# Performance work log

Measured on AMD Instinct MI355X. Metric: run time of the kernel, lower is better.

The kernel has to match this reference:

```python
import jax, jax.numpy as jnp
import numpy as np

B, T, C, H = 8, 1024, 512, 8
EPS = 1e-5


def _layer_norm(x, g, b):
    m = jnp.mean(x, axis=-1, keepdims=True)
    v = jnp.var(x, axis=-1, keepdims=True)
    return (x - m) * jax.lax.rsqrt(v + EPS) * g + b


def setup_inputs() -> dict:
    key = jax.random.key(0)
    ks = jax.random.split(key, 6)
    s = 0.02  # init scale for weights
    return {
        "x": jax.random.normal(ks[0], (B, T, C), dtype=jnp.float32),
        # per-head full-width projections, stacked over heads: [H, C, C]
        "Wq": jax.random.normal(ks[1], (H, C, C), dtype=jnp.float32) * s,
        "bq": jnp.zeros((H, C), dtype=jnp.float32),
        "Wk": jax.random.normal(ks[2], (H, C, C), dtype=jnp.float32) * s,
        "bk": jnp.zeros((H, C), dtype=jnp.float32),
        "Wv": jax.random.normal(ks[3], (H, C, C), dtype=jnp.float32) * s,
        "bv": jnp.zeros((H, C), dtype=jnp.float32),
        # per-head LayerNorm params
        "ln_g": jnp.ones((H, C), dtype=jnp.float32),
        "ln_b": jnp.zeros((H, C), dtype=jnp.float32),
        # output projection: Linear(channels*heads, channels)
        "Wf": jax.random.normal(ks[4], (H * C, C), dtype=jnp.float32) * s,
        "bf": jnp.zeros((C,), dtype=jnp.float32),
    }


def reference(x, Wq, bq, Wk, bk, Wv, bv, ln_g, ln_b, Wf, bf):
    # Batched over heads: the torch code loops heads in Python; here one einsum.
    q = jnp.einsum('btc,hcd->bhtd', x, Wq) + bq[None, :, None, :]
    k = jnp.einsum('btc,hcd->bhtd', x, Wk) + bk[None, :, None, :]
    v = jnp.einsum('btc,hcd->bhtd', x, Wv) + bv[None, :, None, :]
    scale = 1.0 / np.sqrt(C).astype(np.float32)
    attn = jax.nn.softmax(jnp.einsum('bhtd,bhsd->bhts', q, k) * scale, axis=-1)
    z = jnp.einsum('bhts,bhsd->bhtd', attn, v)          # [B,H,T,C]
    z = _layer_norm(z, ln_g[None, :, None, :], ln_b[None, :, None, :])
    # concat heads along feature dim (matches torch.cat(results, dim=-1))
    zc = jnp.transpose(z, (0, 2, 1, 3)).reshape(B, T, H * C)
    out = zc @ Wf + bf + x                               # fc + residual
    return out
```

## Files before the change

kernel.cpp:

```cpp
#include <hip/hip_runtime.h>
#include <hip/hip_bf16.h>
#include <stdint.h>

typedef unsigned short u16;
typedef short s16x8 __attribute__((ext_vector_type(8)));
typedef float f32x4 __attribute__((ext_vector_type(4)));
typedef unsigned short u16x4 __attribute__((ext_vector_type(4)));
typedef unsigned short u16x8 __attribute__((ext_vector_type(8)));

#define B_ 8
#define T_ 1024
#define C_ 512
#define H_ 8
#define M_ (B_*T_)

__device__ __forceinline__ u16 f2bf(float f) {
  unsigned u = __builtin_bit_cast(unsigned, f);
  u += 0x7FFFu + ((u >> 16) & 1u);
  return (u16)(u >> 16);
}

__device__ __forceinline__ f32x4 mfma16(s16x8 a, s16x8 b, f32x4 c) {
  return __builtin_amdgcn_mfma_f32_16x16x32_bf16(a, b, c, 0, 0, 0);
}

__device__ __forceinline__ void glds16(const void* g, void* l) {
  __builtin_amdgcn_global_load_lds(
      (__attribute__((address_space(1))) const uint32_t*)g,
      (__attribute__((address_space(3))) uint32_t*)l, 16, 0, 0);
}

__global__ void cvt_x(const float* __restrict__ src, u16* __restrict__ dst, int n8) {
  int i = blockIdx.x * blockDim.x + threadIdx.x;
  if (i < n8) {
    float4 a = ((const float4*)src)[2*i];
    float4 b = ((const float4*)src)[2*i + 1];
    u16x8 o;
    o[0]=f2bf(a.x); o[1]=f2bf(a.y); o[2]=f2bf(a.z); o[3]=f2bf(a.w);
    o[4]=f2bf(b.x); o[5]=f2bf(b.y); o[6]=f2bf(b.z); o[7]=f2bf(b.w);
    ((u16x8*)dst)[i] = o;
  }
}

__global__ void transpose_f32_to_bf16(const float* __restrict__ src, u16* __restrict__ dst,
                                      int R, int Cc, long sstride, long dstride) {
  int nTc = Cc >> 5;
  int tr = (blockIdx.x / nTc) << 5;
  int tc = (blockIdx.x % nTc) << 5;
  src += (long)blockIdx.y * sstride;
  dst += (long)blockIdx.y * dstride;
  __shared__ float tile[32][33];
  int tx = threadIdx.x, ty = threadIdx.y;
  #pragma unroll
  for (int i = 0; i < 4; ++i) {
    int r = ty + i*8;
    tile[r][tx] = src[(long)(tr + r)*Cc + tc + tx];
  }
  __syncthreads();
  #pragma unroll
  for (int i = 0; i < 4; ++i) {
    int r = ty + i*8;
    dst[(long)(tc + r)*R + tr + tx] = f2bf(tile[tx][r]);
  }
}

#define STAGE_TILE(SRC, STRIDE, LDS)                                        \
  _Pragma("unroll")                                                         \
  for (int r_ = 0; r_ < 4; ++r_) {                                          \
    int o_ = r_*4096 + tid*16;                                              \
    int row_ = o_ >> 7, cb_ = o_ & 127;                                     \
    int cbs_ = cb_ ^ ((row_ & 7) << 4);                                     \
    glds16((SRC) + (size_t)row_*(STRIDE) + kofs + (cbs_ >> 1),              \
           (char*)(LDS) + r_*4096 + ((tid >> 6) << 10));                    \
  }

__global__ __launch_bounds__(256, 2) void gemm_qkv(
    const u16* __restrict__ xbf, const u16* __restrict__ wt,
    const float* __restrict__ bq, const float* __restrict__ bk, const float* __restrict__ bv,
    u16* __restrict__ qO, u16* __restrict__ kO, u16* __restrict__ vT,
    int h0, int lg)
{
  __shared__ u16 As[128*64];
  __shared__ u16 Bs[128*64];
  const int tid = threadIdx.x;
  const int lane = tid & 63, w = tid >> 6;
  const int wm = w >> 1, wn = w & 1;
  const int l15 = lane & 15, l4 = lane >> 4;
  const int by = blockIdx.y;
  const int p = by >> lg;
  const int hh = by & ((1 << lg) - 1);
  const int h = h0 + hh;
  const int ph = p*8 + h;
  const int mt = blockIdx.x >> 2, nt = blockIdx.x & 3;
  const int m0 = mt * 128, n0 = nt * 128;

  const u16* aSrc = xbf + (size_t)m0 * 512;
  const u16* bSrc = wt + ((size_t)ph * 512 + n0) * 512;

  f32x4 acc[4][4];
  #pragma unroll
  for (int i = 0; i < 4; ++i)
    #pragma unroll
    for (int j = 0; j < 4; ++j) acc[i][j] = f32x4{0.f,0.f,0.f,0.f};

  for (int kt = 0; kt < 8; ++kt) {
    const int kofs = kt * 64;
    STAGE_TILE(aSrc, 512, As);
    STAGE_TILE(bSrc, 512, Bs);
    __syncthreads();
    #pragma unroll
    for (int kk = 0; kk < 2; ++kk) {
      s16x8 af[4], bfr[4];
      #pragma unroll
      for (int i = 0; i < 4; ++i) {
        int rowA = wm*64 + i*16 + l15;
        af[i] = *(const s16x8*)((const char*)As + rowA*128 + ((kk*64 + l4*16) ^ ((rowA & 7) << 4)));
        int rowB = wn*64 + i*16 + l15;
        bfr[i] = *(const s16x8*)((const char*)Bs + rowB*128 + ((kk*64 + l4*16) ^ ((rowB & 7) << 4)));
      }
      #pragma unroll
      for (int i = 0; i < 4; ++i)
        #pragma unroll
        for (int j = 0; j < 4; ++j)
          acc[i][j] = mfma16(af[i], bfr[j], acc[i][j]);
    }
    __syncthreads();
  }

  const int dBase = n0 + wn*64;
  const int mBase = m0 + wm*64;
  if (p < 2) {
    const float* bias = (p == 0 ? bq : bk) + h*512;
    u16* outp = (p == 0 ? qO : kO) + (size_t)hh * M_ * 512;
    #pragma unroll
    for (int j = 0; j < 4; ++j) {
      int d = dBase + j*16 + l15;
      float bvs = bias[d];
      #pragma unroll
      for (int i = 0; i < 4; ++i) {
        int m = mBase + i*16 + l4*4;
        #pragma unroll
        for (int r = 0; r < 4; ++r)
          outp[(size_t)(m + r)*512 + d] = f2bf(acc[i][j][r] + bvs);
      }
    }
  } else {
    const float* bias = bv + h*512;
    #pragma unroll
    for (int j = 0; j < 4; ++j) {
      int d = dBase + j*16 + l15;
      float bvs = bias[d];
      #pragma unroll
      for (int i = 0; i < 4; ++i) {
        int m = mBase + i*16 + l4*4;
        int b_ = m >> 10, t0_ = m & 1023;
        u16x4 pk;
        #pragma unroll
        for (int r = 0; r < 4; ++r) pk[r] = f2bf(acc[i][j][r] + bvs);
        *(u16x4*)(vT + (((size_t)(hh*B_ + b_)*512 + d)*1024 + t0_)) = pk;
      }
    }
  }
}

__global__ __launch_bounds__(256, 2) void attn(
    const u16* __restrict__ qB, const u16* __restrict__ kB, const u16* __restrict__ vT,
    const float* __restrict__ lng, const float* __restrict__ lnb,
    u16* __restrict__ zO, int h0)
{
  __shared__ u16 Ks[32*512];
  __shared__ u16 Vs[512*40];
  __shared__ u16 Pl[4][512];
  const int tid = threadIdx.x;
  const int lane = tid & 63, w = tid >> 6;
  const int l15 = lane & 15, l4 = lane >> 4;

  const int Dd = blockIdx.x;
  const int xcd = Dd & 7, slot = Dd >> 3;
  const int gg = xcd + 8*(slot >> 4);
  const int qt = slot & 15;
  const int hg = gg >> 3, b = gg & 7;
  const int h = h0 + hg;
  const int t0 = qt*64 + w*16;
  const size_t hb = (size_t)hg*B_ + b;

  const u16* qP = qB + (hb*1024 + t0 + l15)*512 + l4*8;
  s16x8 qf[16];
  #pragma unroll
  for (int ks = 0; ks < 16; ++ks) qf[ks] = *(const s16x8*)(qP + ks*32);

  f32x4 z[32];
  #pragma unroll
  for (int df = 0; df < 32; ++df) z[df] = f32x4{0.f,0.f,0.f,0.f};
  float L = 0.f;
  const float c1 = 0.06376390696f;

  const u16* kBase = kB + hb*1024*512;
  const u16* vBase = vT + hb*512*1024;
  char* myP = (char*)&Pl[w][0];
  const int swz = (l15 & 3) << 4;
  const int kswz = (l15 & 7) << 4;

  for (int s0 = 0; s0 < 1024; s0 += 32) {
    #pragma unroll
    for (int it = 0; it < 8; ++it) {
      int o = it*4096 + tid*16;
      int row = o >> 10, cb = o & 1023;
      int cbs = cb ^ ((row & 7) << 4);
      glds16(kBase + (size_t)(s0 + row)*512 + (cbs >> 1),
             (char*)Ks + it*4096 + ((tid >> 6) << 10));
    }
    u16x8 vreg[8];
    #pragma unroll
    for (int it = 0; it < 8; ++it) {
      int r = (tid >> 2) + it*64;
      vreg[it] = *(const u16x8*)(vBase + (size_t)r*1024 + s0 + (tid & 3)*8);
    }
    #pragma unroll
    for (int it = 0; it < 8; ++it) {
      int r = (tid >> 2) + it*64;
      *(u16x8*)((char*)Vs + r*80 + (tid & 3)*16) = vreg[it];
    }
    __syncthreads();

    f32x4 sf0 = f32x4{0.f,0.f,0.f,0.f};
    f32x4 sf1 = f32x4{0.f,0.f,0.f,0.f};
    #pragma unroll
    for (int ks = 0; ks < 16; ++ks) {
      int col = (ks*64 + l4*16) ^ kswz;
      s16x8 k0 = *(const s16x8*)((const char*)Ks + l15*1024 + col);
      s16x8 k1 = *(const s16x8*)((const char*)Ks + (16 + l15)*1024 + col);
      sf0 = mfma16(k0, qf[ks], sf0);
      sf1 = mfma16(k1, qf[ks], sf1);
    }
    u16x4 p0, p1;
    #pragma unroll
    for (int r = 0; r < 4; ++r) {
      float e0 = exp2f(sf0[r] * c1);
      float e1 = exp2f(sf1[r] * c1);
      L += e0 + e1;
      p0[r] = f2bf(e0);
      p1[r] = f2bf(e1);
    }
    *(u16x4*)(myP + l15*64 + (( l4*8      ) ^ swz)) = p0;
    *(u16x4*)(myP + l15*64 + ((32 + l4*8  ) ^ swz)) = p1;
    s16x8 pb = *(const s16x8*)(myP + l15*64 + ((l4*16) ^ swz));

    #pragma unroll
    for (int df = 0; df < 32; ++df) {
      int d = df*16 + l15;
      s16x8 va = *(const s16x8*)((const char*)Vs + d*80 + l4*16);
      z[df] = mfma16(va, pb, z[df]);
    }
    __syncthreads();
  }

  L += __shfl_xor(L, 16);
  L += __shfl_xor(L, 32);
  float inv = 1.f / L;

  float s1 = 0.f, s2 = 0.f;
  #pragma unroll
  for (int df = 0; df < 32; ++df)
    #pragma unroll
    for (int r = 0; r < 4; ++r) {
      float v = z[df][r] * inv;
      z[df][r] = v;
      s1 += v; s2 += v*v;
    }
  s1 += __shfl_xor(s1, 16); s1 += __shfl_xor(s1, 32);
  s2 += __shfl_xor(s2, 16); s2 += __shfl_xor(s2, 32);
  const float mean = s1 * (1.f/512.f);
  const float var  = s2 * (1.f/512.f) - mean*mean;
  const float rstd = rsqrtf(var + 1e-5f);

  const float* gp = lng + h*512;
  const float* bp = lnb + h*512;
  u16* zp = zO + ((size_t)(b*1024 + t0 + l15))*4096 + h*512;
  #pragma unroll
  for (int df = 0; df < 32; ++df) {
    int d0 = df*16 + l4*4;
    float4 gv  = *(const float4*)(gp + d0);
    float4 bbv = *(const float4*)(bp + d0);
    u16x4 pk;
    pk[0] = f2bf((z[df][0]-mean)*rstd*gv.x + bbv.x);
    pk[1] = f2bf((z[df][1]-mean)*rstd*gv.y + bbv.y);
    pk[2] = f2bf((z[df][2]-mean)*rstd*gv.z + bbv.z);
    pk[3] = f2bf((z[df][3]-mean)*rstd*gv.w + bbv.w);
    *(u16x4*)(zp + d0) = pk;
  }
}

__global__ __launch_bounds__(256, 2) void gemm_fc(
    const u16* __restrict__ zb, const u16* __restrict__ wft,
    const float* __restrict__ bf_, const float* __restrict__ x,
    float* __restrict__ out)
{
  __shared__ u16 As[128*64];
  __shared__ u16 Bs[128*64];
  const int tid = threadIdx.x;
  const int lane = tid & 63, w = tid >> 6;
  const int wm = w >> 1, wn = w & 1;
  const int l15 = lane & 15, l4 = lane >> 4;
  const int mt = blockIdx.x >> 2, nt = blockIdx.x & 3;
  const int m0 = mt * 128, n0 = nt * 128;

  const u16* aSrc = zb + (size_t)m0 * 4096;
  const u16* bSrc = wft + (size_t)n0 * 4096;

  f32x4 acc[4][4];
  #pragma unroll
  for (int i = 0; i < 4; ++i)
    #pragma unroll
    for (int j = 0; j < 4; ++j) acc[i][j] = f32x4{0.f,0.f,0.f,0.f};

  for (int kt = 0; kt < 64; ++kt) {
    const int kofs = kt * 64;
    STAGE_TILE(aSrc, 4096, As);
    STAGE_TILE(bSrc, 4096, Bs);
    __syncthreads();
    #pragma unroll
    for (int kk = 0; kk < 2; ++kk) {
      s16x8 af[4], bfr[4];
      #pragma unroll
      for (int i = 0; i < 4; ++i) {
        int rowA = wm*64 + i*16 + l15;
        af[i] = *(const s16x8*)((const char*)As + rowA*128 + ((kk*64 + l4*16) ^ ((rowA & 7) << 4)));
        int rowB = wn*64 + i*16 + l15;
        bfr[i] = *(const s16x8*)((const char*)Bs + rowB*128 + ((kk*64 + l4*16) ^ ((rowB & 7) << 4)));
      }
      #pragma unroll
      for (int i = 0; i < 4; ++i)
        #pragma unroll
        for (int j = 0; j < 4; ++j)
          acc[i][j] = mfma16(af[i], bfr[j], acc[i][j]);
    }
    __syncthreads();
  }

  const int dBase = n0 + wn*64;
  const int mBase = m0 + wm*64;
  #pragma unroll
  for (int j = 0; j < 4; ++j) {
    int d = dBase + j*16 + l15;
    float bvs = bf_[d];
    #pragma unroll
    for (int i = 0; i < 4; ++i) {
      int m = mBase + i*16 + l4*4;
      #pragma unroll
      for (int r = 0; r < 4; ++r) {
        size_t idx = (size_t)(m + r)*512 + d;
        out[idx] = acc[i][j][r] + bvs + x[idx];
      }
    }
  }
}

extern "C" void kernel_launch(void* const* d_in, const int* in_sizes, int n_in,
                              void* d_out, int out_size, void* d_ws, size_t ws_size,
                              hipStream_t stream) {
  const float* x   = (const float*)d_in[0];
  const float* Wq  = (const float*)d_in[1];
  const float* bq  = (const float*)d_in[2];
  const float* Wk  = (const float*)d_in[3];
  const float* bk  = (const float*)d_in[4];
  const float* Wv  = (const float*)d_in[5];
  const float* bv  = (const float*)d_in[6];
  const float* lng = (const float*)d_in[7];
  const float* lnb = (const float*)d_in[8];
  const float* Wf  = (const float*)d_in[9];
  const float* bf_ = (const float*)d_in[10];
  float* out = (float*)d_out;

  char* ws = (char*)d_ws;
  u16* xbf = (u16*)(ws);
  u16* wt  = (u16*)(ws + 8388608);
  u16* wft = (u16*)(ws + 20971520);
  u16* zb  = (u16*)(ws + 25165824);

  const size_t headB = 8388608;
  const size_t base  = 92274688;
  int g, lg;
  if      (ws_size >= base + 24*headB) { g = 8; lg = 3; }
  else if (ws_size >= base + 12*headB) { g = 4; lg = 2; }
  else if (ws_size >= base +  6*headB) { g = 2; lg = 1; }
  else                                 { g = 1; lg = 0; }

  u16* qb = (u16*)(ws + base);
  u16* kb = (u16*)(ws + base + (size_t)g*headB);
  u16* vt = (u16*)(ws + base + (size_t)2*g*headB);

  cvt_x<<<2048, 256, 0, stream>>>(x, xbf, 524288);
  dim3 tb(32, 8);
  transpose_f32_to_bf16<<<dim3(256, 8), tb, 0, stream>>>(Wq, wt,             512, 512, 262144, 262144);
  transpose_f32_to_bf16<<<dim3(256, 8), tb, 0, stream>>>(Wk, wt +  8*262144, 512, 512, 262144, 262144);
  transpose_f32_to_bf16<<<dim3(256, 8), tb, 0, stream>>>(Wv, wt + 16*262144, 512, 512, 262144, 262144);
  transpose_f32_to_bf16<<<dim3(2048, 1), tb, 0, stream>>>(Wf, wft, 4096, 512, 0, 0);

  for (int h0 = 0; h0 < H_; h0 += g) {
    gemm_qkv<<<dim3(256, 3*g), 256, 0, stream>>>(xbf, wt, bq, bk, bv, qb, kb, vt, h0, lg);
    attn<<<dim3(128*g), 256, 0, stream>>>(qb, kb, vt, lng, lnb, zb, h0);
  }
  gemm_fc<<<256, 256, 0, stream>>>(zb, wft, bf_, x, out);
}
```

Measured before the change: 685.3 us.

## Double-buffer K/V tiles in attention with async global-to-LDS loads

Splits the K and V shared-memory tiles into two buffers and prefetches the next 32-key tile while the current one is consumed, leaving one barrier per iteration. V is now loaded with direct global-to-LDS copies using an XOR-swizzled layout instead of passing through registers into a padded layout. LDS use roughly doubles, so launch bounds drop to one block per SM, which lowers occupancy in exchange for overlapping memory with compute.

```diff
diff --git a/kernel.cpp b/kernel.cpp
--- a/kernel.cpp
+++ b/kernel.cpp
@@ -163,13 +163,13 @@
   }
 }
 
-__global__ __launch_bounds__(256, 2) void attn(
+__global__ __launch_bounds__(256, 1) void attn(
     const u16* __restrict__ qB, const u16* __restrict__ kB, const u16* __restrict__ vT,
     const float* __restrict__ lng, const float* __restrict__ lnb,
     u16* __restrict__ zO, int h0)
 {
-  __shared__ u16 Ks[32*512];
-  __shared__ u16 Vs[512*40];
+  __shared__ u16 Ks[2][32*512];
+  __shared__ u16 Vs[2][512*32];
   __shared__ u16 Pl[4][512];
   const int tid = threadIdx.x;
   const int lane = tid & 63, w = tid >> 6;
@@ -201,35 +201,44 @@
   const int swz = (l15 & 3) << 4;
   const int kswz = (l15 & 7) << 4;
 
-  for (int s0 = 0; s0 < 1024; s0 += 32) {
+  auto stageK = [&](int buf, int s0) {
     #pragma unroll
     for (int it = 0; it < 8; ++it) {
       int o = it*4096 + tid*16;
       int row = o >> 10, cb = o & 1023;
       int cbs = cb ^ ((row & 7) << 4);
       glds16(kBase + (size_t)(s0 + row)*512 + (cbs >> 1),
-             (char*)Ks + it*4096 + ((tid >> 6) << 10));
-    }
-    u16x8 vreg[8];
+             (char*)Ks[buf] + it*4096 + ((tid >> 6) << 10));
+    }
+  };
+  auto stageV = [&](int buf, int s0) {
     #pragma unroll
     for (int it = 0; it < 8; ++it) {
-      int r = (tid >> 2) + it*64;
-      vreg[it] = *(const u16x8*)(vBase + (size_t)r*1024 + s0 + (tid & 3)*8);
-    }
-    #pragma unroll
-    for (int it = 0; it < 8; ++it) {
-      int r = (tid >> 2) + it*64;
-      *(u16x8*)((char*)Vs + r*80 + (tid & 3)*16) = vreg[it];
-    }
-    __syncthreads();
+      int F = it*4096 + tid*16;
+      int d = F >> 6;
+      int cl = (F & 63) ^ (((d >> 1) & 3) << 4);
+      glds16(vBase + (size_t)d*1024 + s0 + (cl >> 1),
+             (char*)Vs[buf] + it*4096 + ((tid >> 6) << 10));
+    }
+  };
+
+  stageK(0, 0);
+  stageV(0, 0);
+  __syncthreads();
+
+  for (int itr = 0; itr < 32; ++itr) {
+    const int s0 = itr << 5;
+    const int cur = itr & 1;
+    if (itr < 31) { stageK(cur ^ 1, s0 + 32); stageV(cur ^ 1, s0 + 32); }
 
     f32x4 sf0 = f32x4{0.f,0.f,0.f,0.f};
     f32x4 sf1 = f32x4{0.f,0.f,0.f,0.f};
+    const char* ksb = (const char*)Ks[cur];
     #pragma unroll
     for (int ks = 0; ks < 16; ++ks) {
       int col = (ks*64 + l4*16) ^ kswz;
-      s16x8 k0 = *(const s16x8*)((const char*)Ks + l15*1024 + col);
-      s16x8 k1 = *(const s16x8*)((const char*)Ks + (16 + l15)*1024 + col);
+      s16x8 k0 = *(const s16x8*)(ksb + l15*1024 + col);
+      s16x8 k1 = *(const s16x8*)(ksb + (16 + l15)*1024 + col);
       sf0 = mfma16(k0, qf[ks], sf0);
       sf1 = mfma16(k1, qf[ks], sf1);
     }
@@ -246,10 +255,12 @@
     *(u16x4*)(myP + l15*64 + ((32 + l4*8  ) ^ swz)) = p1;
     s16x8 pb = *(const s16x8*)(myP + l15*64 + ((l4*16) ^ swz));
 
+    const char* vsb = (const char*)Vs[cur];
     #pragma unroll
     for (int df = 0; df < 32; ++df) {
       int d = df*16 + l15;
-      s16x8 va = *(const s16x8*)((const char*)Vs + d*80 + l4*16);
+      int off = (d << 6) + ((l4 << 4) ^ (((d >> 1) & 3) << 4));
+      s16x8 va = *(const s16x8*)(vsb + off);
       z[df] = mfma16(va, pb, z[df]);
     }
     __syncthreads();
```

After: 762.2 us. 1.11x slower.
